# Optimization experiments

Measured on AMD Instinct MI355X. Metric: run time of the kernel, lower is better.

## Reference

```python
import jax, jax.numpy as jnp
import numpy as np

N, F_IN, HID, H1, NG = 50000, 128, 64, 4, 512
E = 800000


def setup_inputs() -> dict:
    key = jax.random.key(0)
    ks = jax.random.split(key, 16)
    x = jax.random.normal(ks[0], (N, F_IN), dtype=jnp.float32)
    edge_index = jax.random.randint(ks[1], (2, E), 0, N, dtype=jnp.int64)
    batch = jnp.sort(jax.random.randint(ks[2], (N,), 0, NG, dtype=jnp.int64))
    s = 0.05
    W1 = jax.random.normal(ks[3], (F_IN, H1 * HID), dtype=jnp.float32) * s
    a_src1 = jax.random.normal(ks[4], (H1, HID), dtype=jnp.float32) * s
    a_dst1 = jax.random.normal(ks[5], (H1, HID), dtype=jnp.float32) * s
    b1 = jnp.zeros((H1 * HID,), dtype=jnp.float32)
    W2 = jax.random.normal(ks[6], (H1 * HID, HID), dtype=jnp.float32) * s
    a_src2 = jax.random.normal(ks[7], (1, HID), dtype=jnp.float32) * s
    a_dst2 = jax.random.normal(ks[8], (1, HID), dtype=jnp.float32) * s
    b2 = jnp.zeros((HID,), dtype=jnp.float32)
    Wc = jax.random.normal(ks[9], (HID, 2), dtype=jnp.float32) * s
    bc = jnp.zeros((2,), dtype=jnp.float32)
    return dict(x=x, edge_index=edge_index, batch=batch, W1=W1, a_src1=a_src1,
                a_dst1=a_dst1, b1=b1, W2=W2, a_src2=a_src2, a_dst2=a_dst2,
                b2=b2, Wc=Wc, bc=bc)


def gat_layer(x, W, a_src, a_dst, bias, src, dst, n):
    # PyG GATConv: h = x @ W per head; e_ij = LeakyReLU(a_src.h_j + a_dst.h_i),
    # softmax over incoming edges of each dst node, then scatter-add aggregate.
    H, D = a_src.shape
    h = (x @ W).reshape(n, H, D)                       # [N,H,D]
    asrc = jnp.einsum('nhd,hd->nh', h, a_src)          # [N,H]
    adst = jnp.einsum('nhd,hd->nh', h, a_dst)
    e = jax.nn.leaky_relu(asrc[src] + adst[dst], 0.2)  # [E,H]
    m = jax.lax.stop_gradient(jax.ops.segment_max(e, dst, num_segments=n))
    p = jnp.exp(e - m[dst])
    s = jax.ops.segment_sum(p, dst, num_segments=n)
    alpha = p / (s[dst] + 1e-16)                       # [E,H]
    out = jax.ops.segment_sum(alpha[:, :, None] * h[src], dst, num_segments=n)
    return out.reshape(n, H * D) + bias


def reference(x, edge_index, batch, W1, a_src1, a_dst1, b1, W2, a_src2, a_dst2, b2, Wc, bc):
    n = x.shape[0]
    loops = jnp.arange(n, dtype=edge_index.dtype)
    src = jnp.concatenate([edge_index[0], loops])  # add self-loops (PyG default)
    dst = jnp.concatenate([edge_index[1], loops])
    h = jax.nn.relu(gat_layer(x, W1, a_src1, a_dst1, b1, src, dst, n))
    h = jax.nn.relu(gat_layer(h, W2, a_src2, a_dst2, b2, src, dst, n))
    # global mean pool over graphs
    ng = NG
    sums = jax.ops.segment_sum(h, batch, num_segments=ng)
    cnts = jax.ops.segment_sum(jnp.ones((n,), h.dtype), batch, num_segments=ng)
    pooled = sums / jnp.maximum(cnts, 1.0)[:, None]
    logits = pooled @ Wc + bc
    return jax.nn.log_softmax(logits, axis=1)
```

## Files before the change

### kernel.cpp

```cpp
#include <hip/hip_runtime.h>
#include <hip/hip_bf16.h>
#include <cstddef>
#include <cstdint>

#define FIN   128
#define HID   64
#define H1    4
#define NGRAPH 512
#define BCAP  8192

typedef short bf16x8 __attribute__((ext_vector_type(8)));
typedef float f32x4  __attribute__((ext_vector_type(4)));
typedef float f32x2  __attribute__((ext_vector_type(2)));

#if defined(__has_builtin)
#if __has_builtin(__builtin_amdgcn_cvt_f32_fp8) && __has_builtin(__builtin_amdgcn_cvt_pk_fp8_f32)
#define HAVE_HW_FP8 1
#endif
#if __has_builtin(__builtin_amdgcn_cvt_pk_f32_fp8)
#define HAVE_HW_FP8_PK 1
#endif
#endif

__device__ __forceinline__ float wave_reduce_sum(float v) {
  #pragma unroll
  for (int off = 32; off > 0; off >>= 1) v += __shfl_down(v, off, 64);
  return v;
}

__device__ __forceinline__ float leaky02(float x) {
  return x > 0.0f ? x : 0.2f * x;
}

__device__ __forceinline__ float bf2f(unsigned short u) {
  union { unsigned int i; float f; } v; v.i = ((unsigned int)u) << 16; return v.f;
}
__device__ __forceinline__ unsigned short f2bf(float f) {
  union { float f; unsigned int i; } v; v.f = f;
  unsigned int b = v.i;
  return (unsigned short)((b + 0x7FFFu + ((b >> 16) & 1u)) >> 16);
}

#ifndef HAVE_HW_FP8
__device__ __forceinline__ unsigned char f2fp8_1(float f) {
  unsigned int u = __float_as_uint(f);
  unsigned int s = u >> 31;
  u &= 0x7fffffffu;
  if (u > 0x43e00000u) u = 0x43e00000u;
  unsigned int b = u + (0x0007FFFFu + ((u >> 20) & 1u));
  int e = (int)(b >> 23) - 127;
  unsigned int m = (b >> 20) & 7u;
  unsigned char o;
  if (e < -9) o = 0;
  else if (e < -6) { int sh = -6 - e; o = (unsigned char)((8u | m) >> sh); }
  else if (e > 8) o = 0x7e;
  else o = (unsigned char)(((e + 7) << 3) | m);
  return o | (unsigned char)(s << 7);
}
#endif
__device__ __forceinline__ float fp8tof_1(unsigned char b) {
  unsigned int s = b >> 7, e = (b >> 3) & 15u, m = b & 7u;
  float v = (e == 0) ? (float)m * 0.001953125f
                     : (float)(8u + m) * __uint_as_float((117u + e) << 23);
  return s ? -v : v;
}

__device__ __forceinline__ unsigned char f2fp8(float f) {
#ifdef HAVE_HW_FP8
  return (unsigned char)(__builtin_amdgcn_cvt_pk_fp8_f32(f, f, 0u, false) & 0xffu);
#else
  return f2fp8_1(f);
#endif
}

__device__ __forceinline__ void fma4_fp8(unsigned int hw, float p,
                                         float& a0, float& a1, float& a2, float& a3) {
#ifdef HAVE_HW_FP8_PK
  f32x2 lo = __builtin_amdgcn_cvt_pk_f32_fp8((int)hw, false);
  f32x2 hi = __builtin_amdgcn_cvt_pk_f32_fp8((int)hw, true);
  a0 = fmaf(p, lo.x, a0);
  a1 = fmaf(p, lo.y, a1);
  a2 = fmaf(p, hi.x, a2);
  a3 = fmaf(p, hi.y, a3);
#elif defined(HAVE_HW_FP8)
  a0 = fmaf(p, __builtin_amdgcn_cvt_f32_fp8(hw, 0), a0);
  a1 = fmaf(p, __builtin_amdgcn_cvt_f32_fp8(hw, 1), a1);
  a2 = fmaf(p, __builtin_amdgcn_cvt_f32_fp8(hw, 2), a2);
  a3 = fmaf(p, __builtin_amdgcn_cvt_f32_fp8(hw, 3), a3);
#else
  a0 = fmaf(p, fp8tof_1((unsigned char)(hw & 0xffu)), a0);
  a1 = fmaf(p, fp8tof_1((unsigned char)((hw >> 8) & 0xffu)), a1);
  a2 = fmaf(p, fp8tof_1((unsigned char)((hw >> 16) & 0xffu)), a2);
  a3 = fmaf(p, fp8tof_1((unsigned char)((hw >> 24) & 0xffu)), a3);
#endif
}

#define P3K 8
__global__ __launch_bounds__(256)
void bpart_kernel(const int* __restrict__ src, const int* __restrict__ dst,
                  int* __restrict__ bucketFill, unsigned int* __restrict__ bucketBuf,
                  const float* __restrict__ W1, const float* __restrict__ W2,
                  unsigned short* __restrict__ W1T, unsigned short* __restrict__ W2T,
                  const int* __restrict__ batch, int* __restrict__ gstart,
                  int* __restrict__ gend, int E, int N, int nbuck) {
  int tid = threadIdx.x;
  int stride = gridDim.x * 256;
  int t0 = blockIdx.x * 256 + tid;
  for (int u = t0; u < 256 * 128; u += stride) {
    int n = u >> 7, k = u & 127;
    W1T[u] = f2bf(W1[(size_t)k * 256 + n]);
  }
  for (int u = t0; u < 64 * 256; u += stride) {
    int n = u >> 8, k = u & 255;
    W2T[u] = f2bf(W2[(size_t)k * 64 + n]);
  }
  for (int i = t0; i < N; i += stride) {
    int g = batch[i];
    if (i == 0 || batch[i - 1] != g) gstart[g] = i;
    if (i == N - 1 || batch[i + 1] != g) gend[g] = i + 1;
  }

  __shared__ int lhist[256];
  __shared__ int lbase[256];
  int chunk = 256 * P3K;
  for (int start = blockIdx.x * chunk; start < E; start += gridDim.x * chunk) {
    lhist[tid] = 0;
    __syncthreads();
    int mybuck[P3K]; unsigned int mypack[P3K]; int myrank[P3K];
    #pragma unroll
    for (int k = 0; k < P3K; k++) {
      int i = start + k * 256 + tid;
      if (i < E) {
        int d = dst[i];
        int b = d >> 8;
        mybuck[k] = b;
        mypack[k] = (unsigned int)src[i] | ((unsigned int)(d & 255) << 16);
        myrank[k] = atomicAdd(&lhist[b], 1);
      } else mybuck[k] = -1;
    }
    __syncthreads();
    if (tid < nbuck) lbase[tid] = (lhist[tid] > 0) ? atomicAdd(&bucketFill[tid], lhist[tid]) : 0;
    __syncthreads();
    #pragma unroll
    for (int k = 0; k < P3K; k++) {
      if (mybuck[k] >= 0) {
        int b = mybuck[k];
        int pos = lbase[b] + myrank[k];
        if (pos < BCAP) bucketBuf[((size_t)b << 13) + pos] = mypack[k];
      }
    }
    __syncthreads();
  }
}

__global__ __launch_bounds__(256)
void bbuild_gemm1_kernel(const unsigned int* __restrict__ bucketBuf,
                         const int* __restrict__ bucketFill,
                         int* __restrict__ rowstart, int* __restrict__ rowend,
                         unsigned short* __restrict__ csr,
                         const float* __restrict__ X, const unsigned short* __restrict__ W1T,
                         unsigned char* __restrict__ h1f8,
                         const float* __restrict__ a_src, const float* __restrict__ a_dst,
                         float* __restrict__ asv, float* __restrict__ adv,
                         int N, int nbuck) {
  __shared__ union {
    struct { unsigned short As[64][136]; unsigned short Bs[256][40]; } g;
    struct { int ldeg[256]; int lscan[256]; int lfill[256]; } b;
  } sm;
  int tid = threadIdx.x;

  if (blockIdx.x < (unsigned)nbuck) {
    int b = blockIdx.x;
    int r0 = b << 13;
    int cnt = bucketFill[b]; if (cnt > BCAP) cnt = BCAP;
    int nb0 = b << 8;
    sm.b.ldeg[tid] = 0;
    __syncthreads();
    for (int j = tid; j < cnt; j += 256)
      atomicAdd(&sm.b.ldeg[bucketBuf[r0 + j] >> 16], 1);
    __syncthreads();
    int v = sm.b.ldeg[tid];
    sm.b.lscan[tid] = v;
    __syncthreads();
    for (int off = 1; off < 256; off <<= 1) {
      int u = (tid >= off) ? sm.b.lscan[tid - off] : 0;
      __syncthreads();
      sm.b.lscan[tid] += u;
      __syncthreads();
    }
    int excl = sm.b.lscan[tid] - v;
    sm.b.lfill[tid] = excl;
    if (nb0 + tid < N) {
      rowstart[nb0 + tid] = r0 + excl;
      rowend[nb0 + tid]   = r0 + excl + v;
    }
    __syncthreads();
    for (int j = tid; j < cnt; j += 256) {
      unsigned int p = bucketBuf[r0 + j];
      int pos = r0 + atomicAdd(&sm.b.lfill[p >> 16], 1);
      csr[pos] = (unsigned short)(p & 0xffffu);
    }
    return;
  }

  int t = tid;
  int w = t >> 6, lane = t & 63;
  int quad = lane >> 4, l16 = lane & 15;
  int blockRow = (blockIdx.x - nbuck) * 64;

  {
    int node = t >> 2, kp = (t & 3) * 32;
    int gn = blockRow + node; if (gn >= N) gn = N - 1;
    const float4* xp = (const float4*)(X + (size_t)gn * 128 + kp);
    #pragma unroll
    for (int i = 0; i < 4; i++) {
      float4 va = xp[2 * i], vb = xp[2 * i + 1];
      union { unsigned short u[8]; uint4 v; } r;
      r.u[0] = f2bf(va.x); r.u[1] = f2bf(va.y); r.u[2] = f2bf(va.z); r.u[3] = f2bf(va.w);
      r.u[4] = f2bf(vb.x); r.u[5] = f2bf(vb.y); r.u[6] = f2bf(vb.z); r.u[7] = f2bf(vb.w);
      *(uint4*)&sm.g.As[node][kp + i * 8] = r.v;
    }
  }

  f32x4 acc[4][4];
  #pragma unroll
  for (int i = 0; i < 4; i++)
    #pragma unroll
    for (int j = 0; j < 4; j++) acc[i][j] = (f32x4){0.f, 0.f, 0.f, 0.f};

  for (int kc = 0; kc < FIN; kc += 32) {
    {
      const unsigned short* wp = W1T + (size_t)t * 128 + kc;
      #pragma unroll
      for (int i = 0; i < 4; i++) {
        uint4 v = *(const uint4*)(wp + i * 8);
        *(uint4*)&sm.g.Bs[t][i * 8] = v;
      }
    }
    __syncthreads();
    bf16x8 af[4], bfr[4];
    #pragma unroll
    for (int mt = 0; mt < 4; mt++)
      af[mt] = *(const bf16x8*)&sm.g.As[mt * 16 + l16][kc + quad * 8];
    #pragma unroll
    for (int nt = 0; nt < 4; nt++)
      bfr[nt] = *(const bf16x8*)&sm.g.Bs[w * 64 + nt * 16 + l16][quad * 8];
    #pragma unroll
    for (int mt = 0; mt < 4; mt++)
      #pragma unroll
      for (int nt = 0; nt < 4; nt++)
        acc[mt][nt] = __builtin_amdgcn_mfma_f32_16x16x32_bf16(af[mt], bfr[nt], acc[mt][nt], 0, 0, 0);
    __syncthreads();
  }

  float a_s[4], a_d[4];
  #pragma unroll
  for (int nt = 0; nt < 4; nt++) {
    a_s[nt] = a_src[w * 64 + nt * 16 + l16];
    a_d[nt] = a_dst[w * 64 + nt * 16 + l16];
  }
  #pragma unroll
  for (int mt = 0; mt < 4; mt++) {
    #pragma unroll
    for (int reg = 0; reg < 4; reg++) {
      int node = blockRow + mt * 16 + quad * 4 + reg;
      bool ok = node < N;
      float ps = 0.0f, pd = 0.0f;
      #pragma unroll
      for (int nt = 0; nt < 4; nt++) {
        float v = acc[mt][nt][reg];
        ps = fmaf(v, a_s[nt], ps);
        pd = fmaf(v, a_d[nt], pd);
        if (ok) h1f8[(size_t)node * 256 + w * 64 + nt * 16 + l16] = f2fp8(v);
      }
      #pragma unroll
      for (int off = 8; off > 0; off >>= 1) {
        ps += __shfl_xor(ps, off, 16);
        pd += __shfl_xor(pd, off, 16);
      }
      if (l16 == 0 && ok) {
        asv[(size_t)node * 4 + w] = ps;
        adv[(size_t)node * 4 + w] = pd;
      }
    }
  }
}

__global__ __launch_bounds__(256)
void gemm2_kernel(const unsigned short* __restrict__ out1b, const unsigned short* __restrict__ W2T,
                  unsigned char* __restrict__ h2f8,
                  const float* __restrict__ a_src, const float* __restrict__ a_dst,
                  float* __restrict__ asv, float* __restrict__ adv, int N) {
  __shared__ unsigned short As[64][40];
  __shared__ unsigned short Bs[64][40];
  int t = threadIdx.x;
  int w = t >> 6, lane = t & 63;
  int quad = lane >> 4, l16 = lane & 15;
  int blockRow = blockIdx.x * 64;

  f32x4 acc[4];
  #pragma unroll
  for (int j = 0; j < 4; j++) acc[j] = (f32x4){0.f, 0.f, 0.f, 0.f};

  int nodeS = t >> 2, koff = (t & 3) * 8;
  int gnS = blockRow + nodeS; if (gnS >= N) gnS = N - 1;

  for (int kc = 0; kc < 256; kc += 32) {
    {
      uint4 va = *(const uint4*)(out1b + (size_t)gnS * 256 + kc + koff);
      *(uint4*)&As[nodeS][koff] = va;
      uint4 vb = *(const uint4*)(W2T + (size_t)nodeS * 256 + kc + koff);
      *(uint4*)&Bs[nodeS][koff] = vb;
    }
    __syncthreads();
    bf16x8 af = *(const bf16x8*)&As[w * 16 + l16][quad * 8];
    #pragma unroll
    for (int nt = 0; nt < 4; nt++) {
      bf16x8 bfr = *(const bf16x8*)&Bs[nt * 16 + l16][quad * 8];
      acc[nt] = __builtin_amdgcn_mfma_f32_16x16x32_bf16(af, bfr, acc[nt], 0, 0, 0);
    }
    __syncthreads();
  }

  float a_s[4], a_d[4];
  #pragma unroll
  for (int nt = 0; nt < 4; nt++) {
    a_s[nt] = a_src[nt * 16 + l16];
    a_d[nt] = a_dst[nt * 16 + l16];
  }
  #pragma unroll
  for (int reg = 0; reg < 4; reg++) {
    int node = blockRow + w * 16 + quad * 4 + reg;
    bool ok = node < N;
    float ps = 0.0f, pd = 0.0f;
    #pragma unroll
    for (int nt = 0; nt < 4; nt++) {
      float v = acc[nt][reg];
      ps = fmaf(v, a_s[nt], ps);
      pd = fmaf(v, a_d[nt], pd);
      if (ok) h2f8[(size_t)node * 64 + nt * 16 + l16] = f2fp8(v);
    }
    #pragma unroll
    for (int off = 8; off > 0; off >>= 1) {
      ps += __shfl_xor(ps, off, 16);
      pd += __shfl_xor(pd, off, 16);
    }
    if (l16 == 0 && ok) { asv[node] = ps; adv[node] = pd; }
  }
}

__global__ __launch_bounds__(256)
void agg1_kernel(const unsigned char* __restrict__ h1f8, const int* __restrict__ rowstart,
                 const int* __restrict__ rowend, const unsigned short* __restrict__ csr,
                 const float* __restrict__ asv, const float* __restrict__ adv,
                 const float* __restrict__ b1, unsigned short* __restrict__ out1b, int N) {
  __shared__ int   sbuf[4][64];
  __shared__ float pbuf[4][4][68];
  int wv   = threadIdx.x >> 6;
  int lane = threadIdx.x & 63;
  int n = blockIdx.x * 4 + wv;
  if (n >= N) return;
  int r0 = rowstart[n], r1 = rowend[n];
  float4 ad = *(const float4*)(adv + (size_t)n * 4);
  float4 asn = *(const float4*)(asv + (size_t)n * 4);
  int hsel = lane >> 4;

  float es0 = leaky02(asn.x + ad.x);
  float es1 = leaky02(asn.y + ad.y);
  float es2 = leaky02(asn.z + ad.z);
  float es3 = leaky02(asn.w + ad.w);
  float esel = hsel == 0 ? es0 : (hsel == 1 ? es1 : (hsel == 2 ? es2 : es3));

  float ssum = 0.0f;
  float a0 = 0, a1 = 0, a2 = 0, a3 = 0;

  for (int base = r0; base < r1; base += 64) {
    int j = base + lane;
    int cnt = min(64, r1 - base);
    if (j < r1) {
      int s = csr[j];
      float4 as = *(const float4*)(asv + (size_t)s * 4);
      sbuf[wv][lane] = s;
      pbuf[wv][0][lane] = __expf(leaky02(as.x + ad.x));
      pbuf[wv][1][lane] = __expf(leaky02(as.y + ad.y));
      pbuf[wv][2][lane] = __expf(leaky02(as.z + ad.z));
      pbuf[wv][3][lane] = __expf(leaky02(as.w + ad.w));
    }
    __threadfence_block();

    int c = 0;
    for (; c + 8 <= cnt; c += 8) {
      int4 sv0 = *(const int4*)&sbuf[wv][c];
      int4 sv1 = *(const int4*)&sbuf[wv][c + 4];
      int sc0 = __builtin_amdgcn_readfirstlane(sv0.x);
      int sc1 = __builtin_amdgcn_readfirstlane(sv0.y);
      int sc2 = __builtin_amdgcn_readfirstlane(sv0.z);
      int sc3 = __builtin_amdgcn_readfirstlane(sv0.w);
      int sc4 = __builtin_amdgcn_readfirstlane(sv1.x);
      int sc5 = __builtin_amdgcn_readfirstlane(sv1.y);
      int sc6 = __builtin_amdgcn_readfirstlane(sv1.z);
      int sc7 = __builtin_amdgcn_readfirstlane(sv1.w);
      unsigned int hw0 = *((const unsigned int*)(h1f8 + ((size_t)sc0 << 8)) + lane);
      unsigned int hw1 = *((const unsigned int*)(h1f8 + ((size_t)sc1 << 8)) + lane);
      unsigned int hw2 = *((const unsigned int*)(h1f8 + ((size_t)sc2 << 8)) + lane);
      unsigned int hw3 = *((const unsigned int*)(h1f8 + ((size_t)sc3 << 8)) + lane);
      unsigned int hw4 = *((const unsigned int*)(h1f8 + ((size_t)sc4 << 8)) + lane);
      unsigned int hw5 = *((const unsigned int*)(h1f8 + ((size_t)sc5 << 8)) + lane);
      unsigned int hw6 = *((const unsigned int*)(h1f8 + ((size_t)sc6 << 8)) + lane);
      unsigned int hw7 = *((const unsigned int*)(h1f8 + ((size_t)sc7 << 8)) + lane);
      float4 pva = *(const float4*)&pbuf[wv][hsel][c];
      float4 pvb = *(const float4*)&pbuf[wv][hsel][c + 4];
      ssum += (pva.x + pva.y) + (pva.z + pva.w) + (pvb.x + pvb.y) + (pvb.z + pvb.w);
      fma4_fp8(hw0, pva.x, a0, a1, a2, a3);
      fma4_fp8(hw1, pva.y, a0, a1, a2, a3);
      fma4_fp8(hw2, pva.z, a0, a1, a2, a3);
      fma4_fp8(hw3, pva.w, a0, a1, a2, a3);
      fma4_fp8(hw4, pvb.x, a0, a1, a2, a3);
      fma4_fp8(hw5, pvb.y, a0, a1, a2, a3);
      fma4_fp8(hw6, pvb.z, a0, a1, a2, a3);
      fma4_fp8(hw7, pvb.w, a0, a1, a2, a3);
    }
    for (; c + 4 <= cnt; c += 4) {
      int4 sv = *(const int4*)&sbuf[wv][c];
      int sc0 = __builtin_amdgcn_readfirstlane(sv.x);
      int sc1 = __builtin_amdgcn_readfirstlane(sv.y);
      int sc2 = __builtin_amdgcn_readfirstlane(sv.z);
      int sc3 = __builtin_amdgcn_readfirstlane(sv.w);
      unsigned int hw0 = *((const unsigned int*)(h1f8 + ((size_t)sc0 << 8)) + lane);
      unsigned int hw1 = *((const unsigned int*)(h1f8 + ((size_t)sc1 << 8)) + lane);
      unsigned int hw2 = *((const unsigned int*)(h1f8 + ((size_t)sc2 << 8)) + lane);
      unsigned int hw3 = *((const unsigned int*)(h1f8 + ((size_t)sc3 << 8)) + lane);
      float4 pv = *(const float4*)&pbuf[wv][hsel][c];
      ssum += (pv.x + pv.y) + (pv.z + pv.w);
      fma4_fp8(hw0, pv.x, a0, a1, a2, a3);
      fma4_fp8(hw1, pv.y, a0, a1, a2, a3);
      fma4_fp8(hw2, pv.z, a0, a1, a2, a3);
      fma4_fp8(hw3, pv.w, a0, a1, a2, a3);
    }
    for (; c < cnt; c++) {
      int sc = __builtin_amdgcn_readfirstlane(sbuf[wv][c]);
      float psel = pbuf[wv][hsel][c];
      unsigned int hw = *((const unsigned int*)(h1f8 + ((size_t)sc << 8)) + lane);
      ssum += psel;
      fma4_fp8(hw, psel, a0, a1, a2, a3);
    }
    __threadfence_block();
  }

  {
    float psel = __expf(esel);
    ssum += psel;
    unsigned int hw = *((const unsigned int*)(h1f8 + ((size_t)n << 8)) + lane);
    fma4_fp8(hw, psel, a0, a1, a2, a3);
  }

  float inv = 1.0f / (ssum + 1e-16f);
  int d0 = lane * 4;
  float4 bv = *(const float4*)(b1 + d0);
  float v0 = a0 * inv + bv.x;
  float v1 = a1 * inv + bv.y;
  float v2 = a2 * inv + bv.z;
  float v3 = a3 * inv + bv.w;
  ushort4 o;
  o.x = f2bf(v0 > 0 ? v0 : 0.0f);
  o.y = f2bf(v1 > 0 ? v1 : 0.0f);
  o.z = f2bf(v2 > 0 ? v2 : 0.0f);
  o.w = f2bf(v3 > 0 ? v3 : 0.0f);
  *(ushort4*)(out1b + (size_t)n * 256 + d0) = o;
}

__global__ __launch_bounds__(256)
void agg2_kernel(const unsigned char* __restrict__ h2f8, const int* __restrict__ rowstart,
                 const int* __restrict__ rowend, const unsigned short* __restrict__ csr,
                 const float* __restrict__ asv, const float* __restrict__ adv,
                 const float* __restrict__ b2, unsigned short* __restrict__ h2b, int N) {
  __shared__ int   sbuf[4][64];
  __shared__ float pbuf[4][64];
  int wv   = threadIdx.x >> 6;
  int lane = threadIdx.x & 63;
  int e8 = lane >> 3, l8 = lane & 7;
  int n = blockIdx.x * 4 + wv;
  if (n >= N) return;
  int r0 = rowstart[n], r1 = rowend[n];
  float ad = adv[n];
  float eself = leaky02(asv[n] + ad);
  float q = 0.0f;
  float a0 = 0, a1 = 0, a2 = 0, a3 = 0, a4 = 0, a5 = 0, a6 = 0, a7 = 0;

  for (int base = r0; base < r1; base += 64) {
    int j = base + lane;
    int cnt = min(64, r1 - base);
    if (j < r1) {
      int s = csr[j];
      sbuf[wv][lane] = s;
      pbuf[wv][lane] = __expf(leaky02(asv[s] + ad));
    }
    __threadfence_block();

    int c = 0;
    for (; c + 16 <= cnt; c += 16) {
      int scA = sbuf[wv][c + e8];
      int scB = sbuf[wv][c + 8 + e8];
      float pA = pbuf[wv][c + e8];
      float pB = pbuf[wv][c + 8 + e8];
      uint2 hwA = *(const uint2*)(h2f8 + ((size_t)scA << 6) + l8 * 8);
      uint2 hwB = *(const uint2*)(h2f8 + ((size_t)scB << 6) + l8 * 8);
      q += pA + pB;
      fma4_fp8(hwA.x, pA, a0, a1, a2, a3);
      fma4_fp8(hwA.y, pA, a4, a5, a6, a7);
      fma4_fp8(hwB.x, pB, a0, a1, a2, a3);
      fma4_fp8(hwB.y, pB, a4, a5, a6, a7);
    }
    for (; c + 8 <= cnt; c += 8) {
      int sc = sbuf[wv][c + e8];
      float p1 = pbuf[wv][c + e8];
      uint2 hw = *(const uint2*)(h2f8 + ((size_t)sc << 6) + l8 * 8);
      q += p1;
      fma4_fp8(hw.x, p1, a0, a1, a2, a3);
      fma4_fp8(hw.y, p1, a4, a5, a6, a7);
    }
    int rem = cnt - c;
    if (e8 < rem) {
      int sc = sbuf[wv][c + e8];
      float p1 = pbuf[wv][c + e8];
      uint2 hw = *(const uint2*)(h2f8 + ((size_t)sc << 6) + l8 * 8);
      q += p1;
      fma4_fp8(hw.x, p1, a0, a1, a2, a3);
      fma4_fp8(hw.y, p1, a4, a5, a6, a7);
    }
    __threadfence_block();
  }

  #pragma unroll
  for (int off = 8; off <= 32; off <<= 1) {
    q  += __shfl_xor(q,  off, 64);
    a0 += __shfl_xor(a0, off, 64);
    a1 += __shfl_xor(a1, off, 64);
    a2 += __shfl_xor(a2, off, 64);
    a3 += __shfl_xor(a3, off, 64);
    a4 += __shfl_xor(a4, off, 64);
    a5 += __shfl_xor(a5, off, 64);
    a6 += __shfl_xor(a6, off, 64);
    a7 += __shfl_xor(a7, off, 64);
  }
  float ssum = q;

  {
    float p = __expf(eself);
    ssum += p;
    uint2 hw = *(const uint2*)(h2f8 + ((size_t)n << 6) + l8 * 8);
    fma4_fp8(hw.x, p, a0, a1, a2, a3);
    fma4_fp8(hw.y, p, a4, a5, a6, a7);
  }

  if (e8 == 0) {
    float inv = 1.0f / (ssum + 1e-16f);
    int d0 = l8 * 8;
    float4 bva = *(const float4*)(b2 + d0);
    float4 bvb = *(const float4*)(b2 + d0 + 4);
    float v0 = a0 * inv + bva.x;
    float v1 = a1 * inv + bva.y;
    float v2 = a2 * inv + bva.z;
    float v3 = a3 * inv + bva.w;
    float v4 = a4 * inv + bvb.x;
    float v5 = a5 * inv + bvb.y;
    float v6 = a6 * inv + bvb.z;
    float v7 = a7 * inv + bvb.w;
    union { unsigned short u[8]; uint4 v; } o;
    o.u[0] = f2bf(v0 > 0 ? v0 : 0.0f);
    o.u[1] = f2bf(v1 > 0 ? v1 : 0.0f);
    o.u[2] = f2bf(v2 > 0 ? v2 : 0.0f);
    o.u[3] = f2bf(v3 > 0 ? v3 : 0.0f);
    o.u[4] = f2bf(v4 > 0 ? v4 : 0.0f);
    o.u[5] = f2bf(v5 > 0 ? v5 : 0.0f);
    o.u[6] = f2bf(v6 > 0 ? v6 : 0.0f);
    o.u[7] = f2bf(v7 > 0 ? v7 : 0.0f);
    *(uint4*)(h2b + (size_t)n * 64 + d0) = o.v;
  }
}

__global__ __launch_bounds__(256)
void pool_kernel(const unsigned short* __restrict__ h2b, const int* __restrict__ gstart,
                 const int* __restrict__ gend, const float* __restrict__ Wc,
                 const float* __restrict__ bc, float* __restrict__ out) {
  int g = blockIdx.x;
  int w = threadIdx.x >> 6, lane = threadIdx.x & 63;
  int s = gstart[g], e = gend[g];
  float acc0 = 0.0f, acc1 = 0.0f;
  for (int n = s + w; n < e; n += 4) {
    unsigned int v = *(const unsigned int*)(h2b + (size_t)n * 64 + lane * 2);
    acc0 += __uint_as_float(v << 16);
    acc1 += __uint_as_float(v & 0xffff0000u);
  }
  __shared__ float red0[4][64];
  __shared__ float red1[4][64];
  red0[w][lane] = acc0;
  red1[w][lane] = acc1;
  __syncthreads();
  if (w == 0) {
    float v0 = red0[0][lane] + red0[1][lane] + red0[2][lane] + red0[3][lane];
    float v1 = red1[0][lane] + red1[1][lane] + red1[2][lane] + red1[3][lane];
    float invc = (e > s) ? 1.0f / (float)(e - s) : 0.0f;
    float p0 = v0 * invc, p1 = v1 * invc;
    int d0 = lane * 2;
    float l0 = wave_reduce_sum(fmaf(p0, Wc[d0 * 2 + 0], p1 * Wc[(d0 + 1) * 2 + 0]));
    float l1 = wave_reduce_sum(fmaf(p0, Wc[d0 * 2 + 1], p1 * Wc[(d0 + 1) * 2 + 1]));
    if (lane == 0) {
      l0 += bc[0]; l1 += bc[1];
      float mx = fmaxf(l0, l1);
      float lse = mx + logf(__expf(l0 - mx) + __expf(l1 - mx));
      out[g * 2 + 0] = l0 - lse;
      out[g * 2 + 1] = l1 - lse;
    }
  }
}

extern "C" void kernel_launch(void* const* d_in, const int* in_sizes, int n_in,
                              void* d_out, int out_size, void* d_ws, size_t ws_size,
                              hipStream_t stream) {
  const float* x      = (const float*)d_in[0];
  const int*   ei     = (const int*)d_in[1];
  const int*   batch  = (const int*)d_in[2];
  const float* W1     = (const float*)d_in[3];
  const float* a_src1 = (const float*)d_in[4];
  const float* a_dst1 = (const float*)d_in[5];
  const float* b1     = (const float*)d_in[6];
  const float* W2     = (const float*)d_in[7];
  const float* a_src2 = (const float*)d_in[8];
  const float* a_dst2 = (const float*)d_in[9];
  const float* b2     = (const float*)d_in[10];
  const float* Wc     = (const float*)d_in[11];
  const float* bc     = (const float*)d_in[12];
  float* out = (float*)d_out;

  const int N = in_sizes[0] / FIN;
  const int E = in_sizes[1] / 2;
  const int* srcArr = ei;
  const int* dstArr = ei + E;
  const int nbuck = (N + 255) >> 8;

  char* base = (char*)d_ws;
  size_t off = 0;
  auto alloc = [&](size_t bytes) -> void* {
    void* p = base + off;
    off = (off + bytes + 255) & ~(size_t)255;
    return p;
  };
  unsigned short* W1T  = (unsigned short*)alloc((size_t)256 * 128 * 2);
  unsigned short* W2T  = (unsigned short*)alloc((size_t)64 * 256 * 2);
  unsigned char*  h1f8 = (unsigned char*)alloc((size_t)N * 256);
  unsigned short* out1b= (unsigned short*)alloc((size_t)N * 256 * 2);
  unsigned char*  h2f8 = (unsigned char*)alloc((size_t)N * 64);
  unsigned short* h2b  = (unsigned short*)alloc((size_t)N * 64 * 2);
  float* asv1  = (float*)alloc((size_t)N * 4 * 4);
  float* adv1  = (float*)alloc((size_t)N * 4 * 4);
  float* asv2  = (float*)alloc((size_t)N * 4);
  float* adv2  = (float*)alloc((size_t)N * 4);
  int*   bucketFill= (int*)alloc(256 * 4);
  int*   gstart= (int*)alloc(NGRAPH * 4);
  int*   gend  = (int*)alloc(NGRAPH * 4);
  size_t zspan = (size_t)((char*)gend + NGRAPH * 4 - (char*)bucketFill);
  int*   rowstart = (int*)alloc((size_t)N * 4);
  int*   rowend   = (int*)alloc((size_t)N * 4);
  unsigned int* bucketBuf = (unsigned int*)alloc((size_t)nbuck * BCAP * 4);
  unsigned short* csr = (unsigned short*)alloc((size_t)nbuck * BCAP * 2);
  (void)ws_size; (void)n_in; (void)out_size;

  int gridWv = (N + 3) / 4;
  int gridG  = (N + 63) / 64;
  int gridP3 = (E + 256 * P3K - 1) / (256 * P3K);
  if (gridP3 > 1024) gridP3 = 1024;

  hipMemsetAsync(bucketFill, 0, zspan, stream);
  bpart_kernel<<<gridP3, 256, 0, stream>>>(srcArr, dstArr, bucketFill, bucketBuf,
                                           W1, W2, W1T, W2T, batch, gstart, gend,
                                           E, N, nbuck);
  bbuild_gemm1_kernel<<<nbuck + gridG, 256, 0, stream>>>(
      bucketBuf, bucketFill, rowstart, rowend, csr,
      x, W1T, h1f8, a_src1, a_dst1, asv1, adv1, N, nbuck);
  agg1_kernel<<<gridWv, 256, 0, stream>>>(h1f8, rowstart, rowend, csr, asv1, adv1, b1, out1b, N);

  gemm2_kernel<<<gridG, 256, 0, stream>>>(out1b, W2T, h2f8, a_src2, a_dst2, asv2, adv2, N);
  agg2_kernel<<<gridWv, 256, 0, stream>>>(h2f8, rowstart, rowend, csr, asv2, adv2, b2, h2b, N);

  pool_kernel<<<NGRAPH, 256, 0, stream>>>(h2b, gstart, gend, Wc, bc, out);
}
```

Baseline: 219.6 us.

## Overlap edge partition with GEMM1 and fuse mean-pool into layer-2 aggregation

Moves the weight transpose and graph-boundary setup into a small prep kernel. The edge bucket partition now runs in the same launch as the first GEMM, and the CSR build becomes its own launch, so the partition overlaps the matmul instead of preceding it. Layer-2 aggregation now atomically adds ReLU outputs straight into a per-graph pooled buffer, which removes the bf16 h2 write/read and the pooling pass; a light classify kernel finishes the job. The cost is heavy float atomic contention on 512×64 pooled entries, nondeterministic summation order, and one extra launch.

Measured after the change: 352.8 us. 1.61x slower.

```diff
diff --git a/kernel.cpp b/kernel.cpp
--- a/kernel.cpp
+++ b/kernel.cpp
@@ -95,17 +95,13 @@
 #endif
 }
 
-#define P3K 8
 __global__ __launch_bounds__(256)
-void bpart_kernel(const int* __restrict__ src, const int* __restrict__ dst,
-                  int* __restrict__ bucketFill, unsigned int* __restrict__ bucketBuf,
-                  const float* __restrict__ W1, const float* __restrict__ W2,
-                  unsigned short* __restrict__ W1T, unsigned short* __restrict__ W2T,
-                  const int* __restrict__ batch, int* __restrict__ gstart,
-                  int* __restrict__ gend, int E, int N, int nbuck) {
-  int tid = threadIdx.x;
+void prep_kernel(const float* __restrict__ W1, const float* __restrict__ W2,
+                 unsigned short* __restrict__ W1T, unsigned short* __restrict__ W2T,
+                 const int* __restrict__ batch, int* __restrict__ gstart,
+                 int* __restrict__ gend, int N) {
   int stride = gridDim.x * 256;
-  int t0 = blockIdx.x * 256 + tid;
+  int t0 = blockIdx.x * 256 + threadIdx.x;
   for (int u = t0; u < 256 * 128; u += stride) {
     int n = u >> 7, k = u & 127;
     W1T[u] = f2bf(W1[(size_t)k * 256 + n]);
@@ -119,86 +115,52 @@
     if (i == 0 || batch[i - 1] != g) gstart[g] = i;
     if (i == N - 1 || batch[i + 1] != g) gend[g] = i + 1;
   }
-
-  __shared__ int lhist[256];
-  __shared__ int lbase[256];
-  int chunk = 256 * P3K;
-  for (int start = blockIdx.x * chunk; start < E; start += gridDim.x * chunk) {
-    lhist[tid] = 0;
-    __syncthreads();
-    int mybuck[P3K]; unsigned int mypack[P3K]; int myrank[P3K];
-    #pragma unroll
-    for (int k = 0; k < P3K; k++) {
-      int i = start + k * 256 + tid;
-      if (i < E) {
-        int d = dst[i];
-        int b = d >> 8;
-        mybuck[k] = b;
-        mypack[k] = (unsigned int)src[i] | ((unsigned int)(d & 255) << 16);
-        myrank[k] = atomicAdd(&lhist[b], 1);
-      } else mybuck[k] = -1;
-    }
-    __syncthreads();
-    if (tid < nbuck) lbase[tid] = (lhist[tid] > 0) ? atomicAdd(&bucketFill[tid], lhist[tid]) : 0;
-    __syncthreads();
-    #pragma unroll
-    for (int k = 0; k < P3K; k++) {
-      if (mybuck[k] >= 0) {
-        int b = mybuck[k];
-        int pos = lbase[b] + myrank[k];
-        if (pos < BCAP) bucketBuf[((size_t)b << 13) + pos] = mypack[k];
-      }
-    }
-    __syncthreads();
-  }
-}
-
+}
+
+#define P3K 8
 __global__ __launch_bounds__(256)
-void bbuild_gemm1_kernel(const unsigned int* __restrict__ bucketBuf,
-                         const int* __restrict__ bucketFill,
-                         int* __restrict__ rowstart, int* __restrict__ rowend,
-                         unsigned short* __restrict__ csr,
-                         const float* __restrict__ X, const unsigned short* __restrict__ W1T,
-                         unsigned char* __restrict__ h1f8,
-                         const float* __restrict__ a_src, const float* __restrict__ a_dst,
-                         float* __restrict__ asv, float* __restrict__ adv,
-                         int N, int nbuck) {
+void part_gemm1_kernel(const int* __restrict__ src, const int* __restrict__ dst,
+                       int* __restrict__ bucketFill, unsigned int* __restrict__ bucketBuf,
+                       const float* __restrict__ X, const unsigned short* __restrict__ W1T,
+                       unsigned char* __restrict__ h1f8,
+                       const float* __restrict__ a_src, const float* __restrict__ a_dst,
+                       float* __restrict__ asv, float* __restrict__ adv,
+                       int E, int N, int nbuck, int nPart) {
   __shared__ union {
     struct { unsigned short As[64][136]; unsigned short Bs[256][40]; } g;
-    struct { int ldeg[256]; int lscan[256]; int lfill[256]; } b;
+    struct { int lhist[256]; int lbase[256]; } p;
   } sm;
   int tid = threadIdx.x;
 
-  if (blockIdx.x < (unsigned)nbuck) {
-    int b = blockIdx.x;
-    int r0 = b << 13;
-    int cnt = bucketFill[b]; if (cnt > BCAP) cnt = BCAP;
-    int nb0 = b << 8;
-    sm.b.ldeg[tid] = 0;
-    __syncthreads();
-    for (int j = tid; j < cnt; j += 256)
-      atomicAdd(&sm.b.ldeg[bucketBuf[r0 + j] >> 16], 1);
-    __syncthreads();
-    int v = sm.b.ldeg[tid];
-    sm.b.lscan[tid] = v;
-    __syncthreads();
-    for (int off = 1; off < 256; off <<= 1) {
-      int u = (tid >= off) ? sm.b.lscan[tid - off] : 0;
+  if ((int)blockIdx.x < nPart) {
+    int chunk = 256 * P3K;
+    for (int start = blockIdx.x * chunk; start < E; start += nPart * chunk) {
+      sm.p.lhist[tid] = 0;
       __syncthreads();
-      sm.b.lscan[tid] += u;
+      int mybuck[P3K]; unsigned int mypack[P3K]; int myrank[P3K];
+      #pragma unroll
+      for (int k = 0; k < P3K; k++) {
+        int i = start + k * 256 + tid;
+        if (i < E) {
+          int d = dst[i];
+          int b = d >> 8;
+          mybuck[k] = b;
+          mypack[k] = (unsigned int)src[i] | ((unsigned int)(d & 255) << 16);
+          myrank[k] = atomicAdd(&sm.p.lhist[b], 1);
+        } else mybuck[k] = -1;
+      }
       __syncthreads();
-    }
-    int excl = sm.b.lscan[tid] - v;
-    sm.b.lfill[tid] = excl;
-    if (nb0 + tid < N) {
-      rowstart[nb0 + tid] = r0 + excl;
-      rowend[nb0 + tid]   = r0 + excl + v;
-    }
-    __syncthreads();
-    for (int j = tid; j < cnt; j += 256) {
-      unsigned int p = bucketBuf[r0 + j];
-      int pos = r0 + atomicAdd(&sm.b.lfill[p >> 16], 1);
-      csr[pos] = (unsigned short)(p & 0xffffu);
+      if (tid < nbuck) sm.p.lbase[tid] = (sm.p.lhist[tid] > 0) ? atomicAdd(&bucketFill[tid], sm.p.lhist[tid]) : 0;
+      __syncthreads();
+      #pragma unroll
+      for (int k = 0; k < P3K; k++) {
+        if (mybuck[k] >= 0) {
+          int b = mybuck[k];
+          int pos = sm.p.lbase[b] + myrank[k];
+          if (pos < BCAP) bucketBuf[((size_t)b << 13) + pos] = mypack[k];
+        }
+      }
+      __syncthreads();
     }
     return;
   }
@@ -206,7 +168,7 @@
   int t = tid;
   int w = t >> 6, lane = t & 63;
   int quad = lane >> 4, l16 = lane & 15;
-  int blockRow = (blockIdx.x - nbuck) * 64;
+  int blockRow = (blockIdx.x - nPart) * 64;
 
   {
     int node = t >> 2, kp = (t & 3) * 32;
@@ -283,6 +245,47 @@
         adv[(size_t)node * 4 + w] = pd;
       }
     }
+  }
+}
+
+__global__ __launch_bounds__(256)
+void bbuild_kernel(const unsigned int* __restrict__ bucketBuf,
+                   const int* __restrict__ bucketFill,
+                   int* __restrict__ rowstart, int* __restrict__ rowend,
+                   unsigned short* __restrict__ csr, int N) {
+  __shared__ int ldeg[256];
+  __shared__ int lscan[256];
+  __shared__ int lfill[256];
+  int tid = threadIdx.x;
+  int b = blockIdx.x;
+  int r0 = b << 13;
+  int cnt = bucketFill[b]; if (cnt > BCAP) cnt = BCAP;
+  int nb0 = b << 8;
+  ldeg[tid] = 0;
+  __syncthreads();
+  for (int j = tid; j < cnt; j += 256)
+    atomicAdd(&ldeg[bucketBuf[r0 + j] >> 16], 1);
+  __syncthreads();
+  int v = ldeg[tid];
+  lscan[tid] = v;
+  __syncthreads();
+  for (int off = 1; off < 256; off <<= 1) {
+    int u = (tid >= off) ? lscan[tid - off] : 0;
+    __syncthreads();
+    lscan[tid] += u;
+    __syncthreads();
+  }
+  int excl = lscan[tid] - v;
+  lfill[tid] = excl;
+  if (nb0 + tid < N) {
+    rowstart[nb0 + tid] = r0 + excl;
+    rowend[nb0 + tid]   = r0 + excl + v;
+  }
+  __syncthreads();
+  for (int j = tid; j < cnt; j += 256) {
+    unsigned int p = bucketBuf[r0 + j];
+    int pos = r0 + atomicAdd(&lfill[p >> 16], 1);
+    csr[pos] = (unsigned short)(p & 0xffffu);
   }
 }
 
@@ -473,7 +476,8 @@
 void agg2_kernel(const unsigned char* __restrict__ h2f8, const int* __restrict__ rowstart,
                  const int* __restrict__ rowend, const unsigned short* __restrict__ csr,
                  const float* __restrict__ asv, const float* __restrict__ adv,
-                 const float* __restrict__ b2, unsigned short* __restrict__ h2b, int N) {
+                 const float* __restrict__ b2, const int* __restrict__ batch,
+                 float* __restrict__ pooled, int N) {
   __shared__ int   sbuf[4][64];
   __shared__ float pbuf[4][64];
   int wv   = threadIdx.x >> 6;
@@ -558,60 +562,45 @@
     int d0 = l8 * 8;
     float4 bva = *(const float4*)(b2 + d0);
     float4 bvb = *(const float4*)(b2 + d0 + 4);
-    float v0 = a0 * inv + bva.x;
-    float v1 = a1 * inv + bva.y;
-    float v2 = a2 * inv + bva.z;
-    float v3 = a3 * inv + bva.w;
-    float v4 = a4 * inv + bvb.x;
-    float v5 = a5 * inv + bvb.y;
-    float v6 = a6 * inv + bvb.z;
-    float v7 = a7 * inv + bvb.w;
-    union { unsigned short u[8]; uint4 v; } o;
-    o.u[0] = f2bf(v0 > 0 ? v0 : 0.0f);
-    o.u[1] = f2bf(v1 > 0 ? v1 : 0.0f);
-    o.u[2] = f2bf(v2 > 0 ? v2 : 0.0f);
-    o.u[3] = f2bf(v3 > 0 ? v3 : 0.0f);
-    o.u[4] = f2bf(v4 > 0 ? v4 : 0.0f);
-    o.u[5] = f2bf(v5 > 0 ? v5 : 0.0f);
-    o.u[6] = f2bf(v6 > 0 ? v6 : 0.0f);
-    o.u[7] = f2bf(v7 > 0 ? v7 : 0.0f);
-    *(uint4*)(h2b + (size_t)n * 64 + d0) = o.v;
+    float v0 = fmaxf(a0 * inv + bva.x, 0.0f);
+    float v1 = fmaxf(a1 * inv + bva.y, 0.0f);
+    float v2 = fmaxf(a2 * inv + bva.z, 0.0f);
+    float v3 = fmaxf(a3 * inv + bva.w, 0.0f);
+    float v4 = fmaxf(a4 * inv + bvb.x, 0.0f);
+    float v5 = fmaxf(a5 * inv + bvb.y, 0.0f);
+    float v6 = fmaxf(a6 * inv + bvb.z, 0.0f);
+    float v7 = fmaxf(a7 * inv + bvb.w, 0.0f);
+    int g = batch[n];
+    float* pg = pooled + ((size_t)g << 6) + d0;
+    atomicAdd(pg + 0, v0);
+    atomicAdd(pg + 1, v1);
+    atomicAdd(pg + 2, v2);
+    atomicAdd(pg + 3, v3);
+    atomicAdd(pg + 4, v4);
+    atomicAdd(pg + 5, v5);
+    atomicAdd(pg + 6, v6);
+    atomicAdd(pg + 7, v7);
   }
 }
 
 __global__ __launch_bounds__(256)
-void pool_kernel(const unsigned short* __restrict__ h2b, const int* __restrict__ gstart,
-                 const int* __restrict__ gend, const float* __restrict__ Wc,
-                 const float* __restrict__ bc, float* __restrict__ out) {
-  int g = blockIdx.x;
-  int w = threadIdx.x >> 6, lane = threadIdx.x & 63;
-  int s = gstart[g], e = gend[g];
-  float acc0 = 0.0f, acc1 = 0.0f;
-  for (int n = s + w; n < e; n += 4) {
-    unsigned int v = *(const unsigned int*)(h2b + (size_t)n * 64 + lane * 2);
-    acc0 += __uint_as_float(v << 16);
-    acc1 += __uint_as_float(v & 0xffff0000u);
-  }
-  __shared__ float red0[4][64];
-  __shared__ float red1[4][64];
-  red0[w][lane] = acc0;
-  red1[w][lane] = acc1;
-  __syncthreads();
-  if (w == 0) {
-    float v0 = red0[0][lane] + red0[1][lane] + red0[2][lane] + red0[3][lane];
-    float v1 = red1[0][lane] + red1[1][lane] + red1[2][lane] + red1[3][lane];
-    float invc = (e > s) ? 1.0f / (float)(e - s) : 0.0f;
-    float p0 = v0 * invc, p1 = v1 * invc;
-    int d0 = lane * 2;
-    float l0 = wave_reduce_sum(fmaf(p0, Wc[d0 * 2 + 0], p1 * Wc[(d0 + 1) * 2 + 0]));
-    float l1 = wave_reduce_sum(fmaf(p0, Wc[d0 * 2 + 1], p1 * Wc[(d0 + 1) * 2 + 1]));
-    if (lane == 0) {
-      l0 += bc[0]; l1 += bc[1];
-      float mx = fmaxf(l0, l1);
-      float lse = mx + logf(__expf(l0 - mx) + __expf(l1 - mx));
-      out[g * 2 + 0] = l0 - lse;
-      out[g * 2 + 1] = l1 - lse;
-    }
+void classify_kernel(const float* __restrict__ pooled, const int* __restrict__ gstart,
+                     const int* __restrict__ gend, const float* __restrict__ Wc,
+                     const float* __restrict__ bc, float* __restrict__ out, int ngraph) {
+  int wv = threadIdx.x >> 6, lane = threadIdx.x & 63;
+  int g = blockIdx.x * 4 + wv;
+  if (g >= ngraph) return;
+  int cnt = gend[g] - gstart[g];
+  float invc = cnt > 0 ? 1.0f / (float)cnt : 0.0f;
+  float p = pooled[((size_t)g << 6) + lane] * invc;
+  float l0 = wave_reduce_sum(p * Wc[lane * 2 + 0]);
+  float l1 = wave_reduce_sum(p * Wc[lane * 2 + 1]);
+  if (lane == 0) {
+    l0 += bc[0]; l1 += bc[1];
+    float mx = fmaxf(l0, l1);
+    float lse = mx + logf(__expf(l0 - mx) + __expf(l1 - mx));
+    out[g * 2 + 0] = l0 - lse;
+    out[g * 2 + 1] = l1 - lse;
   }
 }
 
@@ -651,7 +640,6 @@
   unsigned char*  h1f8 = (unsigned char*)alloc((size_t)N * 256);
   unsigned short* out1b= (unsigned short*)alloc((size_t)N * 256 * 2);
   unsigned char*  h2f8 = (unsigned char*)alloc((size_t)N * 64);
-  unsigned short* h2b  = (unsigned short*)alloc((size_t)N * 64 * 2);
   float* asv1  = (float*)alloc((size_t)N * 4 * 4);
   float* adv1  = (float*)alloc((size_t)N * 4 * 4);
   float* asv2  = (float*)alloc((size_t)N * 4);
@@ -659,7 +647,8 @@
   int*   bucketFill= (int*)alloc(256 * 4);
   int*   gstart= (int*)alloc(NGRAPH * 4);
   int*   gend  = (int*)alloc(NGRAPH * 4);
-  size_t zspan = (size_t)((char*)gend + NGRAPH * 4 - (char*)bucketFill);
+  float* pooled= (float*)alloc((size_t)NGRAPH * 64 * 4);
+  size_t zspan = (size_t)((char*)pooled + (size_t)NGRAPH * 64 * 4 - (char*)bucketFill);
   int*   rowstart = (int*)alloc((size_t)N * 4);
   int*   rowend   = (int*)alloc((size_t)N * 4);
   unsigned int* bucketBuf = (unsigned int*)alloc((size_t)nbuck * BCAP * 4);
@@ -668,20 +657,20 @@
 
   int gridWv = (N + 3) / 4;
   int gridG  = (N + 63) / 64;
-  int gridP3 = (E + 256 * P3K - 1) / (256 * P3K);
-  if (gridP3 > 1024) gridP3 = 1024;
+  int nPart  = (E + 256 * P3K - 1) / (256 * P3K);
+  if (nPart > 1024) nPart = 1024;
 
   hipMemsetAsync(bucketFill, 0, zspan, stream);
-  bpart_kernel<<<gridP3, 256, 0, stream>>>(srcArr, dstArr, bucketFill, bucketBuf,
-                                           W1, W2, W1T, W2T, batch, gstart, gend,
-                                           E, N, nbuck);
-  bbuild_gemm1_kernel<<<nbuck + gridG, 256, 0, stream>>>(
-      bucketBuf, bucketFill, rowstart, rowend, csr,
-      x, W1T, h1f8, a_src1, a_dst1, asv1, adv1, N, nbuck);
+  prep_kernel<<<512, 256, 0, stream>>>(W1, W2, W1T, W2T, batch, gstart, gend, N);
+  part_gemm1_kernel<<<nPart + gridG, 256, 0, stream>>>(
+      srcArr, dstArr, bucketFill, bucketBuf,
+      x, W1T, h1f8, a_src1, a_dst1, asv1, adv1, E, N, nbuck, nPart);
+  bbuild_kernel<<<nbuck, 256, 0, stream>>>(bucketBuf, bucketFill, rowstart, rowend, csr, N);
   agg1_kernel<<<gridWv, 256, 0, stream>>>(h1f8, rowstart, rowend, csr, asv1, adv1, b1, out1b, N);
 
   gemm2_kernel<<<gridG, 256, 0, stream>>>(out1b, W2T, h2f8, a_src2, a_dst2, asv2, adv2, N);
-  agg2_kernel<<<gridWv, 256, 0, stream>>>(h2f8, rowstart, rowend, csr, asv2, adv2, b2, h2b, N);
-
-  pool_kernel<<<NGRAPH, 256, 0, stream>>>(h2b, gstart, gend, Wc, bc, out);
-}
+  agg2_kernel<<<gridWv, 256, 0, stream>>>(h2f8, rowstart, rowend, csr, asv2, adv2, b2,
+                                          batch, pooled, N);
+
+  classify_kernel<<<(NGRAPH + 3) / 4, 256, 0, stream>>>(pooled, gstart, gend, Wc, bc, out, NGRAPH);
+}
```

## Co-schedule edge partitioning with GEMM1 and split bucket build into own kernel

Applied to the files above, without the earlier changes.

Weight transposition and graph-boundary detection move into a small prep kernel. Edge bucket partitioning now runs in the same launch as the layer-1 GEMM, so the two can overlap. Bucket-to-CSR building becomes its own kernel that runs after that launch. This changes the launch count from two to three before agg1 in exchange for overlapping the atomic-heavy partition with compute-bound GEMM blocks.

After: 224.9 us. 2.4% more time.

```diff
diff --git a/kernel.cpp b/kernel.cpp
--- a/kernel.cpp
+++ b/kernel.cpp
@@ -95,17 +95,13 @@
 #endif
 }
 
-#define P3K 8
 __global__ __launch_bounds__(256)
-void bpart_kernel(const int* __restrict__ src, const int* __restrict__ dst,
-                  int* __restrict__ bucketFill, unsigned int* __restrict__ bucketBuf,
-                  const float* __restrict__ W1, const float* __restrict__ W2,
-                  unsigned short* __restrict__ W1T, unsigned short* __restrict__ W2T,
-                  const int* __restrict__ batch, int* __restrict__ gstart,
-                  int* __restrict__ gend, int E, int N, int nbuck) {
-  int tid = threadIdx.x;
+void prep_kernel(const float* __restrict__ W1, const float* __restrict__ W2,
+                 unsigned short* __restrict__ W1T, unsigned short* __restrict__ W2T,
+                 const int* __restrict__ batch, int* __restrict__ gstart,
+                 int* __restrict__ gend, int N) {
   int stride = gridDim.x * 256;
-  int t0 = blockIdx.x * 256 + tid;
+  int t0 = blockIdx.x * 256 + threadIdx.x;
   for (int u = t0; u < 256 * 128; u += stride) {
     int n = u >> 7, k = u & 127;
     W1T[u] = f2bf(W1[(size_t)k * 256 + n]);
@@ -119,86 +115,52 @@
     if (i == 0 || batch[i - 1] != g) gstart[g] = i;
     if (i == N - 1 || batch[i + 1] != g) gend[g] = i + 1;
   }
-
-  __shared__ int lhist[256];
-  __shared__ int lbase[256];
-  int chunk = 256 * P3K;
-  for (int start = blockIdx.x * chunk; start < E; start += gridDim.x * chunk) {
-    lhist[tid] = 0;
-    __syncthreads();
-    int mybuck[P3K]; unsigned int mypack[P3K]; int myrank[P3K];
-    #pragma unroll
-    for (int k = 0; k < P3K; k++) {
-      int i = start + k * 256 + tid;
-      if (i < E) {
-        int d = dst[i];
-        int b = d >> 8;
-        mybuck[k] = b;
-        mypack[k] = (unsigned int)src[i] | ((unsigned int)(d & 255) << 16);
-        myrank[k] = atomicAdd(&lhist[b], 1);
-      } else mybuck[k] = -1;
-    }
-    __syncthreads();
-    if (tid < nbuck) lbase[tid] = (lhist[tid] > 0) ? atomicAdd(&bucketFill[tid], lhist[tid]) : 0;
-    __syncthreads();
-    #pragma unroll
-    for (int k = 0; k < P3K; k++) {
-      if (mybuck[k] >= 0) {
-        int b = mybuck[k];
-        int pos = lbase[b] + myrank[k];
-        if (pos < BCAP) bucketBuf[((size_t)b << 13) + pos] = mypack[k];
-      }
-    }
-    __syncthreads();
-  }
-}
-
+}
+
+#define P3K 8
 __global__ __launch_bounds__(256)
-void bbuild_gemm1_kernel(const unsigned int* __restrict__ bucketBuf,
-                         const int* __restrict__ bucketFill,
-                         int* __restrict__ rowstart, int* __restrict__ rowend,
-                         unsigned short* __restrict__ csr,
-                         const float* __restrict__ X, const unsigned short* __restrict__ W1T,
-                         unsigned char* __restrict__ h1f8,
-                         const float* __restrict__ a_src, const float* __restrict__ a_dst,
-                         float* __restrict__ asv, float* __restrict__ adv,
-                         int N, int nbuck) {
+void part_gemm1_kernel(const int* __restrict__ src, const int* __restrict__ dst,
+                       int* __restrict__ bucketFill, unsigned int* __restrict__ bucketBuf,
+                       const float* __restrict__ X, const unsigned short* __restrict__ W1T,
+                       unsigned char* __restrict__ h1f8,
+                       const float* __restrict__ a_src, const float* __restrict__ a_dst,
+                       float* __restrict__ asv, float* __restrict__ adv,
+                       int E, int N, int nbuck, int nPart) {
   __shared__ union {
     struct { unsigned short As[64][136]; unsigned short Bs[256][40]; } g;
-    struct { int ldeg[256]; int lscan[256]; int lfill[256]; } b;
+    struct { int lhist[256]; int lbase[256]; } p;
   } sm;
   int tid = threadIdx.x;
 
-  if (blockIdx.x < (unsigned)nbuck) {
-    int b = blockIdx.x;
-    int r0 = b << 13;
-    int cnt = bucketFill[b]; if (cnt > BCAP) cnt = BCAP;
-    int nb0 = b << 8;
-    sm.b.ldeg[tid] = 0;
-    __syncthreads();
-    for (int j = tid; j < cnt; j += 256)
-      atomicAdd(&sm.b.ldeg[bucketBuf[r0 + j] >> 16], 1);
-    __syncthreads();
-    int v = sm.b.ldeg[tid];
-    sm.b.lscan[tid] = v;
-    __syncthreads();
-    for (int off = 1; off < 256; off <<= 1) {
-      int u = (tid >= off) ? sm.b.lscan[tid - off] : 0;
+  if ((int)blockIdx.x < nPart) {
+    int chunk = 256 * P3K;
+    for (int start = blockIdx.x * chunk; start < E; start += nPart * chunk) {
+      sm.p.lhist[tid] = 0;
       __syncthreads();
-      sm.b.lscan[tid] += u;
+      int mybuck[P3K]; unsigned int mypack[P3K]; int myrank[P3K];
+      #pragma unroll
+      for (int k = 0; k < P3K; k++) {
+        int i = start + k * 256 + tid;
+        if (i < E) {
+          int d = dst[i];
+          int b = d >> 8;
+          mybuck[k] = b;
+          mypack[k] = (unsigned int)src[i] | ((unsigned int)(d & 255) << 16);
+          myrank[k] = atomicAdd(&sm.p.lhist[b], 1);
+        } else mybuck[k] = -1;
+      }
       __syncthreads();
-    }
-    int excl = sm.b.lscan[tid] - v;
-    sm.b.lfill[tid] = excl;
-    if (nb0 + tid < N) {
-      rowstart[nb0 + tid] = r0 + excl;
-      rowend[nb0 + tid]   = r0 + excl + v;
-    }
-    __syncthreads();
-    for (int j = tid; j < cnt; j += 256) {
-      unsigned int p = bucketBuf[r0 + j];
-      int pos = r0 + atomicAdd(&sm.b.lfill[p >> 16], 1);
-      csr[pos] = (unsigned short)(p & 0xffffu);
+      if (tid < nbuck) sm.p.lbase[tid] = (sm.p.lhist[tid] > 0) ? atomicAdd(&bucketFill[tid], sm.p.lhist[tid]) : 0;
+      __syncthreads();
+      #pragma unroll
+      for (int k = 0; k < P3K; k++) {
+        if (mybuck[k] >= 0) {
+          int b = mybuck[k];
+          int pos = sm.p.lbase[b] + myrank[k];
+          if (pos < BCAP) bucketBuf[((size_t)b << 13) + pos] = mypack[k];
+        }
+      }
+      __syncthreads();
     }
     return;
   }
@@ -206,7 +168,7 @@
   int t = tid;
   int w = t >> 6, lane = t & 63;
   int quad = lane >> 4, l16 = lane & 15;
-  int blockRow = (blockIdx.x - nbuck) * 64;
+  int blockRow = (blockIdx.x - nPart) * 64;
 
   {
     int node = t >> 2, kp = (t & 3) * 32;
@@ -283,6 +245,47 @@
         adv[(size_t)node * 4 + w] = pd;
       }
     }
+  }
+}
+
+__global__ __launch_bounds__(256)
+void bbuild_kernel(const unsigned int* __restrict__ bucketBuf,
+                   const int* __restrict__ bucketFill,
+                   int* __restrict__ rowstart, int* __restrict__ rowend,
+                   unsigned short* __restrict__ csr, int N) {
+  __shared__ int ldeg[256];
+  __shared__ int lscan[256];
+  __shared__ int lfill[256];
+  int tid = threadIdx.x;
+  int b = blockIdx.x;
+  int r0 = b << 13;
+  int cnt = bucketFill[b]; if (cnt > BCAP) cnt = BCAP;
+  int nb0 = b << 8;
+  ldeg[tid] = 0;
+  __syncthreads();
+  for (int j = tid; j < cnt; j += 256)
+    atomicAdd(&ldeg[bucketBuf[r0 + j] >> 16], 1);
+  __syncthreads();
+  int v = ldeg[tid];
+  lscan[tid] = v;
+  __syncthreads();
+  for (int off = 1; off < 256; off <<= 1) {
+    int u = (tid >= off) ? lscan[tid - off] : 0;
+    __syncthreads();
+    lscan[tid] += u;
+    __syncthreads();
+  }
+  int excl = lscan[tid] - v;
+  lfill[tid] = excl;
+  if (nb0 + tid < N) {
+    rowstart[nb0 + tid] = r0 + excl;
+    rowend[nb0 + tid]   = r0 + excl + v;
+  }
+  __syncthreads();
+  for (int j = tid; j < cnt; j += 256) {
+    unsigned int p = bucketBuf[r0 + j];
+    int pos = r0 + atomicAdd(&lfill[p >> 16], 1);
+    csr[pos] = (unsigned short)(p & 0xffffu);
   }
 }
 
@@ -668,16 +671,15 @@
 
   int gridWv = (N + 3) / 4;
   int gridG  = (N + 63) / 64;
-  int gridP3 = (E + 256 * P3K - 1) / (256 * P3K);
-  if (gridP3 > 1024) gridP3 = 1024;
+  int nPart  = (E + 256 * P3K - 1) / (256 * P3K);
+  if (nPart > 1024) nPart = 1024;
 
   hipMemsetAsync(bucketFill, 0, zspan, stream);
-  bpart_kernel<<<gridP3, 256, 0, stream>>>(srcArr, dstArr, bucketFill, bucketBuf,
-                                           W1, W2, W1T, W2T, batch, gstart, gend,
-                                           E, N, nbuck);
-  bbuild_gemm1_kernel<<<nbuck + gridG, 256, 0, stream>>>(
-      bucketBuf, bucketFill, rowstart, rowend, csr,
-      x, W1T, h1f8, a_src1, a_dst1, asv1, adv1, N, nbuck);
+  prep_kernel<<<512, 256, 0, stream>>>(W1, W2, W1T, W2T, batch, gstart, gend, N);
+  part_gemm1_kernel<<<nPart + gridG, 256, 0, stream>>>(
+      srcArr, dstArr, bucketFill, bucketBuf,
+      x, W1T, h1f8, a_src1, a_dst1, asv1, adv1, E, N, nbuck, nPart);
+  bbuild_kernel<<<nbuck, 256, 0, stream>>>(bucketBuf, bucketFill, rowstart, rowend, csr, N);
   agg1_kernel<<<gridWv, 256, 0, stream>>>(h1f8, rowstart, rowend, csr, asv1, adv1, b1, out1b, N);
 
   gemm2_kernel<<<gridG, 256, 0, stream>>>(out1b, W2T, h2f8, a_src2, a_dst2, asv2, adv2, N);
```
